# Kernel optimization log

Measured on AMD Instinct MI355X. Metric: run time of the kernel, lower is better.

## Reference

```python
import jax, jax.numpy as jnp
import numpy as np

N = 50000
E = 400000
IN_DIM = 256
H1 = 512
H2 = 128
P_DROP = 0.5


def setup_inputs() -> dict:
    key = jax.random.key(0)
    ks = jax.random.split(key, 8)
    x = jax.random.normal(ks[0], (N, IN_DIM), dtype=jnp.float32)
    edge_index = jax.random.randint(ks[1], (2, E), 0, N, dtype=jnp.int64)
    W1 = jax.random.normal(ks[2], (IN_DIM, H1), dtype=jnp.float32) * (1.0 / np.sqrt(IN_DIM))
    b1 = jnp.zeros((H1,), dtype=jnp.float32)
    W2 = jax.random.normal(ks[3], (H1, H2), dtype=jnp.float32) * (1.0 / np.sqrt(H1))
    b2 = jnp.zeros((H2,), dtype=jnp.float32)
    a = jnp.full((1,), 0.25, dtype=jnp.float32)  # PReLU default init
    mask1 = jax.random.bernoulli(ks[4], 1.0 - P_DROP, (N, H1))
    mask2 = jax.random.bernoulli(ks[5], 1.0 - P_DROP, (N, H2))
    return {"x": x, "edge_index": edge_index, "W1": W1, "b1": b1,
            "W2": W2, "b2": b2, "a": a, "mask1": mask1, "mask2": mask2}


def reference(x, edge_index, W1, b1, W2, b2, a, mask1, mask2):
    n = x.shape[0]
    loop = jnp.arange(n, dtype=edge_index.dtype)
    src = jnp.concatenate([edge_index[0], loop])  # [E+N] with self-loops
    dst = jnp.concatenate([edge_index[1], loop])
    # symmetric normalization: deg^-1/2[src] * deg^-1/2[dst]
    deg = jax.ops.segment_sum(jnp.ones(src.shape[0], x.dtype), dst, num_segments=n)
    dis = jnp.where(deg > 0, jax.lax.rsqrt(jnp.maximum(deg, 1.0)), 0.0)
    norm = dis[src] * dis[dst]  # [E+N]

    scale = 1.0 / (1.0 - P_DROP)

    def gcn_conv(h, W, b):
        h = h @ W                               # dense transform [n, out]
        msg = h[src] * norm[:, None]            # gather + normalize [E+N, out]
        return jax.ops.segment_sum(msg, dst, num_segments=n) + b

    def prelu_dropout(h, mask):
        h = jnp.where(h >= 0, h, a * h)         # PReLU (shared scalar a)
        return jnp.where(mask, h * scale, 0.0)  # dropout p=0.5

    feat1 = prelu_dropout(gcn_conv(x, W1, b1), mask1)
    feat2 = prelu_dropout(gcn_conv(feat1, W2, b2), mask2)
    return feat2
```

## Files before the change

### kernel.cpp

```cpp
#include <hip/hip_runtime.h>
#include <hip/hip_bf16.h>

#define IN_DIM 256
#define H1 512
#define H2 128
#define BM 128
#define BKK 64
#define LDT 72
#define SCAN_CHUNK 4096

typedef unsigned short u16;
typedef unsigned long long u64;
typedef __attribute__((ext_vector_type(8))) short short8;
typedef __attribute__((ext_vector_type(4))) float floatx4;

__device__ __forceinline__ u16 f2bf(float f) {
    union { float f; unsigned u; } c; c.f = f;
    unsigned u = c.u;
    return (u16)((u + 0x7fffu + ((u >> 16) & 1u)) >> 16);
}
__device__ __forceinline__ float bflo(unsigned w) {
    union { unsigned u; float f; } c; c.u = w << 16; return c.f;
}
__device__ __forceinline__ float bfhi(unsigned w) {
    union { unsigned u; float f; } c; c.u = w & 0xffff0000u; return c.f;
}


__global__ __launch_bounds__(256) void prep_kernel(const int4* __restrict__ mask4,
        u64* __restrict__ bits, int total4,
        const int* __restrict__ dstA, int* __restrict__ counts, int E, int n,
        const float* __restrict__ W1, u16* __restrict__ w1t,
        const float* __restrict__ W2, u16* __restrict__ w2t,
        int PB, int HB, int T1B) {
    int b = blockIdx.x;
    if (b < PB) {
        int gid = b * 256 + threadIdx.x;
        int lane = threadIdx.x & 63;
        int4 v = (gid < total4) ? mask4[gid] : make_int4(0, 0, 0, 0);
        u64 b0 = __ballot(v.x != 0);
        u64 b1 = __ballot(v.y != 0);
        u64 b2 = __ballot(v.z != 0);
        u64 b3 = __ballot(v.w != 0);
        u64 sel = (lane == 0) ? b0 : (lane == 1) ? b1 : (lane == 2) ? b2 : b3;
        if (lane < 4 && gid < total4)
            bits[(size_t)(gid >> 6) * 4 + lane] = sel;
    } else if (b < PB + HB) {
        int e = (b - PB) * 256 + threadIdx.x;
        if (e < E) {
            int d = dstA[e];
            if ((unsigned)d < (unsigned)n) atomicAdd(&counts[d], 1);
        }
    } else if (b < PB + HB + T1B) {
        int idx = (b - PB - HB) * 256 + threadIdx.x;
        if (idx < IN_DIM * H1) {
            int k = idx >> 9, c = idx & (H1 - 1);
            w1t[c * IN_DIM + k] = f2bf(W1[idx]);
        }
    } else {
        int idx = (b - PB - HB - T1B) * 256 + threadIdx.x;
        if (idx < H1 * H2) {
            int k = idx >> 7, c = idx & (H2 - 1);
            w2t[c * H1 + k] = f2bf(W2[idx]);
        }
    }
}


__global__ __launch_bounds__(256) void partial_sum_kernel(const int* __restrict__ counts,
        int* __restrict__ partials, int n) {
    int t = threadIdx.x;
    int base = blockIdx.x * SCAN_CHUNK + t * 16;
    int s = 0;
    int m = (base < n) ? min(16, n - base) : 0;
    for (int i = 0; i < m; ++i) s += (counts[base + i] + 1) & ~1;
    __shared__ int red[256];
    red[t] = s;
    __syncthreads();
    for (int off = 128; off > 0; off >>= 1) {
        if (t < off) red[t] += red[t + off];
        __syncthreads();
    }
    if (t == 0) partials[blockIdx.x] = red[0];
}

__global__ void scan_partials_kernel(int* __restrict__ partials, int nb,
                                     unsigned* __restrict__ ts_zero_row) {
    int t = threadIdx.x;
    if (t < 64) ts_zero_row[t] = 0;
    if (t == 0 && blockIdx.x == 0) {
        int run = 0;
        for (int i = 0; i < nb; ++i) { int c = partials[i]; partials[i] = run; run += c; }
        partials[nb] = run;
    }
}

__global__ __launch_bounds__(256) void scan_emit_kernel(const int* __restrict__ counts,
        const int* __restrict__ partials, int* __restrict__ row_start,
        int* __restrict__ cursor, float* __restrict__ dis,
        int* __restrict__ csr, int n, int nb) {
    int t = threadIdx.x;
    int base = blockIdx.x * SCAN_CHUNK + t * 16;
    int cnt[16];
    int s = 0;
    int m = (base < n) ? min(16, n - base) : 0;
    for (int i = 0; i < m; ++i) { cnt[i] = counts[base + i]; s += (cnt[i] + 1) & ~1; }
    __shared__ int red[256];
    red[t] = s;
    __syncthreads();
    for (int off = 1; off < 256; off <<= 1) {
        int v = red[t];
        int vo = (t >= off) ? red[t - off] : 0;
        __syncthreads();
        red[t] = v + vo;
        __syncthreads();
    }
    int run = partials[blockIdx.x] + (t ? red[t - 1] : 0);
    for (int i = 0; i < m; ++i) {
        int c = cnt[i];
        row_start[base + i] = run;
        cursor[base + i] = run;
        dis[base + i] = rsqrtf((float)(c + 1));
        if (c & 1) csr[run + c] = n;
        run += (c + 1) & ~1;
    }
    if (blockIdx.x == 0 && t == 0) row_start[n] = partials[nb];
}

__global__ void scatter_kernel(const int* __restrict__ srcA, const int* __restrict__ dstA,
                               int* __restrict__ cursor, int* __restrict__ csr,
                               int E, int n) {
    int e = blockIdx.x * blockDim.x + threadIdx.x;
    if (e < E) {
        int d = dstA[e];
        int s = srcA[e];
        if ((unsigned)d < (unsigned)n && (unsigned)s < (unsigned)n) {
            int p = atomicAdd(&cursor[d], 1);
            csr[p] = s;
        }
    }
}

__global__ void scale_cast_kernel(const float* __restrict__ x, const float* __restrict__ dis,
                                  u16* __restrict__ xs, int n) {
    int gid = blockIdx.x * blockDim.x + threadIdx.x;
    int total = (n + 1) * (IN_DIM / 4);
    if (gid >= total) return;
    int node = gid >> 6;
    uint2 o = make_uint2(0, 0);
    if (node < n) {
        float4 v = ((const float4*)x)[gid];
        float d = dis[node];
        o.x = (unsigned)f2bf(v.x * d) | ((unsigned)f2bf(v.y * d) << 16);
        o.y = (unsigned)f2bf(v.z * d) | ((unsigned)f2bf(v.w * d) << 16);
    }
    ((uint2*)xs)[gid] = o;
}


__global__ __launch_bounds__(256) void agg1_kernel(const u16* __restrict__ xs,
        const int* __restrict__ row_start, const int* __restrict__ csr,
        const float* __restrict__ dis, u16* __restrict__ aggx, int n) {
    int gid = blockIdx.x * blockDim.x + threadIdx.x;
    int w = gid >> 6, lane = gid & 63;
    if (w >= n) return;
    const uint4* base = (const uint4*)xs;
    int half = lane >> 5, hl = lane & 31;
    float a0 = 0.f, a1 = 0.f, a2 = 0.f, a3 = 0.f, a4 = 0.f, a5 = 0.f, a6 = 0.f, a7 = 0.f;
    if (half == 0) {
        uint4 u = base[(size_t)w * 32 + hl];
        a0 = bflo(u.x); a1 = bfhi(u.x); a2 = bflo(u.y); a3 = bfhi(u.y);
        a4 = bflo(u.z); a5 = bfhi(u.z); a6 = bflo(u.w); a7 = bfhi(u.w);
    }
    int b = row_start[w], e = row_start[w + 1];
    int i = b;
    for (; i + 8 <= e; i += 8) {
        int s0 = csr[i + half],     s1 = csr[i + 2 + half];
        int s2 = csr[i + 4 + half], s3 = csr[i + 6 + half];
        uint4 u0 = base[(size_t)s0 * 32 + hl];
        uint4 u1 = base[(size_t)s1 * 32 + hl];
        uint4 u2 = base[(size_t)s2 * 32 + hl];
        uint4 u3 = base[(size_t)s3 * 32 + hl];
        a0 += (bflo(u0.x) + bflo(u1.x)) + (bflo(u2.x) + bflo(u3.x));
        a1 += (bfhi(u0.x) + bfhi(u1.x)) + (bfhi(u2.x) + bfhi(u3.x));
        a2 += (bflo(u0.y) + bflo(u1.y)) + (bflo(u2.y) + bflo(u3.y));
        a3 += (bfhi(u0.y) + bfhi(u1.y)) + (bfhi(u2.y) + bfhi(u3.y));
        a4 += (bflo(u0.z) + bflo(u1.z)) + (bflo(u2.z) + bflo(u3.z));
        a5 += (bfhi(u0.z) + bfhi(u1.z)) + (bfhi(u2.z) + bfhi(u3.z));
        a6 += (bflo(u0.w) + bflo(u1.w)) + (bflo(u2.w) + bflo(u3.w));
        a7 += (bfhi(u0.w) + bfhi(u1.w)) + (bfhi(u2.w) + bfhi(u3.w));
    }
    for (; i < e; i += 2) {
        int s = csr[i + half];
        uint4 u = base[(size_t)s * 32 + hl];
        a0 += bflo(u.x); a1 += bfhi(u.x); a2 += bflo(u.y); a3 += bfhi(u.y);
        a4 += bflo(u.z); a5 += bfhi(u.z); a6 += bflo(u.w); a7 += bfhi(u.w);
    }
    a0 += __shfl_xor(a0, 32); a1 += __shfl_xor(a1, 32);
    a2 += __shfl_xor(a2, 32); a3 += __shfl_xor(a3, 32);
    a4 += __shfl_xor(a4, 32); a5 += __shfl_xor(a5, 32);
    a6 += __shfl_xor(a6, 32); a7 += __shfl_xor(a7, 32);
    if (half == 0) {
        float dd = dis[w];
        uint4 o;
        o.x = (unsigned)f2bf(a0 * dd) | ((unsigned)f2bf(a1 * dd) << 16);
        o.y = (unsigned)f2bf(a2 * dd) | ((unsigned)f2bf(a3 * dd) << 16);
        o.z = (unsigned)f2bf(a4 * dd) | ((unsigned)f2bf(a5 * dd) << 16);
        o.w = (unsigned)f2bf(a6 * dd) | ((unsigned)f2bf(a7 * dd) << 16);
        ((uint4*)aggx)[(size_t)w * 32 + hl] = o;
    }
}


__global__ __launch_bounds__(256) void gemm1_kernel(const u16* __restrict__ A,
        const u16* __restrict__ Bt, const float* __restrict__ bias,
        const float* __restrict__ a_p, const u64* __restrict__ mbits,
        u16* __restrict__ out, int M) {
    const int K = IN_DIM;
    __shared__ __align__(16) u16 As[BM * LDT];
    __shared__ __align__(16) u16 Bs[BM * LDT];
    int tid = threadIdx.x;
    int wave = tid >> 6, lane = tid & 63;
    int quad = lane >> 4, l16 = lane & 15;
    int wm = wave & 1, wn = wave >> 1;
    int m0 = blockIdx.x * BM, n0 = blockIdx.y * BM;

    floatx4 acc[4][4];
#pragma unroll
    for (int i = 0; i < 4; i++)
#pragma unroll
        for (int j = 0; j < 4; j++) acc[i][j] = (floatx4){0.f, 0.f, 0.f, 0.f};

    for (int k0 = 0; k0 < K; k0 += BKK) {
        __syncthreads();
#pragma unroll
        for (int u = tid; u < 1024; u += 256) {
            int row = u >> 3, seg = u & 7;
            uint4 av = make_uint4(0, 0, 0, 0);
            int gr = m0 + row;
            if (gr < M) av = *(const uint4*)&A[(size_t)gr * K + k0 + seg * 8];
            *(uint4*)&As[row * LDT + seg * 8] = av;
            uint4 bv = *(const uint4*)&Bt[(size_t)(n0 + row) * K + k0 + seg * 8];
            *(uint4*)&Bs[row * LDT + seg * 8] = bv;
        }
        __syncthreads();
        short8 bf8[4][2];
#pragma unroll
        for (int i = 0; i < 4; i++)
#pragma unroll
            for (int ks = 0; ks < 2; ks++)
                bf8[i][ks] = *(const short8*)&Bs[(wn * 64 + i * 16 + l16) * LDT + ks * 32 + quad * 8];
#pragma unroll
        for (int mt = 0; mt < 4; mt++) {
            short8 af0 = *(const short8*)&As[(wm * 64 + mt * 16 + l16) * LDT + quad * 8];
            short8 af1 = *(const short8*)&As[(wm * 64 + mt * 16 + l16) * LDT + 32 + quad * 8];
#pragma unroll
            for (int nt = 0; nt < 4; nt++) {
                acc[mt][nt] = __builtin_amdgcn_mfma_f32_16x16x32_bf16(
                    af0, bf8[nt][0], acc[mt][nt], 0, 0, 0);
                acc[mt][nt] = __builtin_amdgcn_mfma_f32_16x16x32_bf16(
                    af1, bf8[nt][1], acc[mt][nt], 0, 0, 0);
            }
        }
    }

    u64* mb = (u64*)As;
    __syncthreads();
    for (int u = tid; u < BM * 4; u += 256) {
        int row = u >> 2, j = u & 3;
        int gr = m0 + row;
        u64 val = 0;
        if (gr < M) val = mbits[(size_t)gr * 8 + (n0 >> 8) * 4 + j];
        mb[row * 5 + j] = val;
    }
    __syncthreads();

    float alpha = a_p[0];
#pragma unroll
    for (int mt = 0; mt < 4; mt++) {
#pragma unroll
        for (int r = 0; r < 4; r++) {
            int lr = wm * 64 + mt * 16 + quad * 4 + r;
            int row = m0 + lr;
            if (row >= M) continue;
#pragma unroll
            for (int nt = 0; nt < 4; nt++) {
                int c64 = nt * 16 + l16;
                int col = n0 + wn * 64 + c64;
                float v = acc[mt][nt][r] + bias[col];
                v = (v >= 0.f) ? v : alpha * v;
                u64 w = mb[lr * 5 + (l16 & 3)];
                int bit = ((n0 >> 2) + wn * 16 + nt * 4 + (l16 >> 2)) & 63;
                v = ((w >> bit) & 1ull) ? v * 2.0f : 0.0f;
                out[(size_t)row * H1 + col] = f2bf(v);
            }
        }
    }
}


__global__ __launch_bounds__(256) void gemm2_kernel(const u16* __restrict__ A,
        const u16* __restrict__ Bt, const float* __restrict__ dis,
        u16* __restrict__ out, int M) {
    const int K = H1;
    __shared__ __align__(16) u16 As[64 * LDT];
    __shared__ __align__(16) u16 Bs[128 * LDT];
    int tid = threadIdx.x;
    int wave = tid >> 6, lane = tid & 63;
    int quad = lane >> 4, l16 = lane & 15;
    int wm = wave & 1, wn = wave >> 1;
    int m0 = blockIdx.x * 64;

    floatx4 acc[2][4];
#pragma unroll
    for (int i = 0; i < 2; i++)
#pragma unroll
        for (int j = 0; j < 4; j++) acc[i][j] = (floatx4){0.f, 0.f, 0.f, 0.f};

    for (int k0 = 0; k0 < K; k0 += BKK) {
        __syncthreads();
#pragma unroll
        for (int u = tid; u < 1536; u += 256) {
            if (u < 512) {
                int row = u >> 3, seg = u & 7;
                uint4 av = make_uint4(0, 0, 0, 0);
                int gr = m0 + row;
                if (gr < M) av = *(const uint4*)&A[(size_t)gr * K + k0 + seg * 8];
                *(uint4*)&As[row * LDT + seg * 8] = av;
            } else {
                int v2 = u - 512;
                int row = v2 >> 3, seg = v2 & 7;
                uint4 bv = *(const uint4*)&Bt[(size_t)row * K + k0 + seg * 8];
                *(uint4*)&Bs[row * LDT + seg * 8] = bv;
            }
        }
        __syncthreads();
        short8 bf8[4][2];
#pragma unroll
        for (int i = 0; i < 4; i++)
#pragma unroll
            for (int ks = 0; ks < 2; ks++)
                bf8[i][ks] = *(const short8*)&Bs[(wn * 64 + i * 16 + l16) * LDT + ks * 32 + quad * 8];
#pragma unroll
        for (int mt = 0; mt < 2; mt++) {
            short8 af0 = *(const short8*)&As[(wm * 32 + mt * 16 + l16) * LDT + quad * 8];
            short8 af1 = *(const short8*)&As[(wm * 32 + mt * 16 + l16) * LDT + 32 + quad * 8];
#pragma unroll
            for (int nt = 0; nt < 4; nt++) {
                acc[mt][nt] = __builtin_amdgcn_mfma_f32_16x16x32_bf16(
                    af0, bf8[nt][0], acc[mt][nt], 0, 0, 0);
                acc[mt][nt] = __builtin_amdgcn_mfma_f32_16x16x32_bf16(
                    af1, bf8[nt][1], acc[mt][nt], 0, 0, 0);
            }
        }
    }

#pragma unroll
    for (int mt = 0; mt < 2; mt++) {
#pragma unroll
        for (int r = 0; r < 4; r++) {
            int row = m0 + wm * 32 + mt * 16 + quad * 4 + r;
            if (row >= M) continue;
            float dd = dis[row];
#pragma unroll
            for (int nt = 0; nt < 4; nt++) {
                int col = wn * 64 + nt * 16 + l16;
                out[(size_t)row * H2 + col] = f2bf(acc[mt][nt][r] * dd);
            }
        }
    }
}


__global__ __launch_bounds__(256) void agg2_kernel(const u16* __restrict__ ts,
        const int* __restrict__ row_start, const int* __restrict__ csr,
        const float* __restrict__ dis, const float* __restrict__ b2,
        const float* __restrict__ a_p, const int* __restrict__ mask,
        float* __restrict__ out, int n) {
    int gid = blockIdx.x * blockDim.x + threadIdx.x;
    int w = gid >> 6, lane = gid & 63;
    if (w >= n) return;
    const uint2* base = (const uint2*)ts;
    int half = lane >> 5, hl = lane & 31;
    float a0 = 0.f, a1 = 0.f, a2 = 0.f, a3 = 0.f;
    if (half == 0) {
        uint2 u = base[(size_t)w * 32 + hl];
        a0 = bflo(u.x); a1 = bfhi(u.x); a2 = bflo(u.y); a3 = bfhi(u.y);
    }
    int b = row_start[w], e = row_start[w + 1];
    int i = b;
    for (; i + 8 <= e; i += 8) {
        int s0 = csr[i + half],     s1 = csr[i + 2 + half];
        int s2 = csr[i + 4 + half], s3 = csr[i + 6 + half];
        uint2 u0 = base[(size_t)s0 * 32 + hl];
        uint2 u1 = base[(size_t)s1 * 32 + hl];
        uint2 u2 = base[(size_t)s2 * 32 + hl];
        uint2 u3 = base[(size_t)s3 * 32 + hl];
        a0 += (bflo(u0.x) + bflo(u1.x)) + (bflo(u2.x) + bflo(u3.x));
        a1 += (bfhi(u0.x) + bfhi(u1.x)) + (bfhi(u2.x) + bfhi(u3.x));
        a2 += (bflo(u0.y) + bflo(u1.y)) + (bflo(u2.y) + bflo(u3.y));
        a3 += (bfhi(u0.y) + bfhi(u1.y)) + (bfhi(u2.y) + bfhi(u3.y));
    }
    for (; i < e; i += 2) {
        int s = csr[i + half];
        uint2 u = base[(size_t)s * 32 + hl];
        a0 += bflo(u.x); a1 += bfhi(u.x); a2 += bflo(u.y); a3 += bfhi(u.y);
    }
    a0 += __shfl_xor(a0, 32); a1 += __shfl_xor(a1, 32);
    a2 += __shfl_xor(a2, 32); a3 += __shfl_xor(a3, 32);
    if (half == 0) {
        float dd = dis[w];
        float alpha = a_p[0];
        float4 bb = ((const float4*)b2)[hl];
        float v0 = dd * a0 + bb.x;
        float v1 = dd * a1 + bb.y;
        float v2 = dd * a2 + bb.z;
        float v3 = dd * a3 + bb.w;
        v0 = (v0 >= 0.f) ? v0 : alpha * v0;
        v1 = (v1 >= 0.f) ? v1 : alpha * v1;
        v2 = (v2 >= 0.f) ? v2 : alpha * v2;
        v3 = (v3 >= 0.f) ? v3 : alpha * v3;
        int4 m = ((const int4*)mask)[(size_t)w * 32 + hl];
        v0 = m.x ? v0 * 2.f : 0.f;
        v1 = m.y ? v1 * 2.f : 0.f;
        v2 = m.z ? v2 * 2.f : 0.f;
        v3 = m.w ? v3 * 2.f : 0.f;
        ((float4*)out)[(size_t)w * 32 + hl] = make_float4(v0, v1, v2, v3);
    }
}


extern "C" void kernel_launch(void* const* d_in, const int* in_sizes, int n_in,
                              void* d_out, int out_size, void* d_ws, size_t ws_size,
                              hipStream_t stream) {
    const float* x  = (const float*)d_in[0];
    const int* ei   = (const int*)d_in[1];
    const float* W1 = (const float*)d_in[2];
    const float* b1 = (const float*)d_in[3];
    const float* W2 = (const float*)d_in[4];
    const float* b2 = (const float*)d_in[5];
    const float* ap = (const float*)d_in[6];
    const int* mask1 = (const int*)d_in[7];
    const int* mask2 = (const int*)d_in[8];

    int n = in_sizes[0] / IN_DIM;
    int E = in_sizes[1] / 2;
    const int* srcA = ei;
    const int* dstA = ei + E;

    char* p = (char*)d_ws;
    auto alloc = [&](size_t bytes) {
        char* r = p;
        p += (bytes + 255) & ~(size_t)255;
        return r;
    };
    u16* feat1     = (u16*)alloc((size_t)n * H1 * 2);
    u16* xs        = feat1;
    u16* ts        = (u16*)alloc((size_t)(n + 1) * H2 * 2);
    u64* bits1     = (u64*)ts;
    u16* w1t       = (u16*)alloc((size_t)IN_DIM * H1 * 2);
    u16* w2t       = (u16*)alloc((size_t)H1 * H2 * 2);
    float* dis     = (float*)alloc((size_t)n * 4);
    int* counts    = (int*)alloc((size_t)n * 4);
    int* cursor    = (int*)alloc((size_t)n * 4);
    int* row_start = (int*)alloc(((size_t)n + 1) * 4);
    int* csr       = (int*)alloc(((size_t)E + n + 64) * 4);
    int nscan = (n + SCAN_CHUNK - 1) / SCAN_CHUNK;
    int* partials  = (int*)alloc(((size_t)nscan + 1) * 4);
    u16* aggx      = (u16*)d_out;
    if ((size_t)(p - (char*)d_ws) > ws_size) return;

    const int tpb = 256;
    int total4 = n * H1 / 4;
    int PB = (total4 + tpb - 1) / tpb;
    int HB = (E + tpb - 1) / tpb;
    int T1B = (IN_DIM * H1 + tpb - 1) / tpb;
    int T2B = (H1 * H2 + tpb - 1) / tpb;
    hipMemsetAsync(counts, 0, (size_t)n * 4, stream);
    prep_kernel<<<PB + HB + T1B + T2B, tpb, 0, stream>>>((const int4*)mask1, bits1, total4,
        dstA, counts, E, n, W1, w1t, W2, w2t, PB, HB, T1B);
    partial_sum_kernel<<<nscan, tpb, 0, stream>>>(counts, partials, n);
    scan_partials_kernel<<<1, 64, 0, stream>>>(partials, nscan,
        (unsigned*)(ts + (size_t)n * H2));
    scan_emit_kernel<<<nscan, tpb, 0, stream>>>(counts, partials, row_start, cursor, dis,
                                                csr, n, nscan);
    scatter_kernel<<<(E + tpb - 1) / tpb, tpb, 0, stream>>>(srcA, dstA, cursor, csr, E, n);
    scale_cast_kernel<<<(((n + 1) * (IN_DIM / 4)) + tpb - 1) / tpb, tpb, 0, stream>>>(x, dis, xs, n);
    agg1_kernel<<<(n * 64 + tpb - 1) / tpb, tpb, 0, stream>>>(xs, row_start, csr, dis, aggx, n);
    dim3 g1((n + BM - 1) / BM, H1 / BM);
    gemm1_kernel<<<g1, tpb, 0, stream>>>(aggx, w1t, b1, ap, bits1, feat1, n);
    dim3 g2((n + 63) / 64, 1);
    gemm2_kernel<<<g2, tpb, 0, stream>>>(feat1, w2t, dis, ts, n);
    agg2_kernel<<<(n * 64 + tpb - 1) / tpb, tpb, 0, stream>>>(ts, row_start, csr, dis, b2, ap,
                                                              mask2, (float*)d_out, n);
}
```

Baseline: 408.4 us.

## Load GEMM MFMA fragments directly from global memory instead of LDS staging

```diff
diff --git a/kernel.cpp b/kernel.cpp
--- a/kernel.cpp
+++ b/kernel.cpp
@@ -5,8 +5,6 @@
 #define H1 512
 #define H2 128
 #define BM 128
-#define BKK 64
-#define LDT 72
 #define SCAN_CHUNK 4096
 
 typedef unsigned short u16;
@@ -217,55 +215,13 @@
         const float* __restrict__ a_p, const u64* __restrict__ mbits,
         u16* __restrict__ out, int M) {
     const int K = IN_DIM;
-    __shared__ __align__(16) u16 As[BM * LDT];
-    __shared__ __align__(16) u16 Bs[BM * LDT];
+    __shared__ u64 mb[BM * 5];
     int tid = threadIdx.x;
     int wave = tid >> 6, lane = tid & 63;
     int quad = lane >> 4, l16 = lane & 15;
     int wm = wave & 1, wn = wave >> 1;
     int m0 = blockIdx.x * BM, n0 = blockIdx.y * BM;
 
-    floatx4 acc[4][4];
-#pragma unroll
-    for (int i = 0; i < 4; i++)
-#pragma unroll
-        for (int j = 0; j < 4; j++) acc[i][j] = (floatx4){0.f, 0.f, 0.f, 0.f};
-
-    for (int k0 = 0; k0 < K; k0 += BKK) {
-        __syncthreads();
-#pragma unroll
-        for (int u = tid; u < 1024; u += 256) {
-            int row = u >> 3, seg = u & 7;
-            uint4 av = make_uint4(0, 0, 0, 0);
-            int gr = m0 + row;
-            if (gr < M) av = *(const uint4*)&A[(size_t)gr * K + k0 + seg * 8];
-            *(uint4*)&As[row * LDT + seg * 8] = av;
-            uint4 bv = *(const uint4*)&Bt[(size_t)(n0 + row) * K + k0 + seg * 8];
-            *(uint4*)&Bs[row * LDT + seg * 8] = bv;
-        }
-        __syncthreads();
-        short8 bf8[4][2];
-#pragma unroll
-        for (int i = 0; i < 4; i++)
-#pragma unroll
-            for (int ks = 0; ks < 2; ks++)
-                bf8[i][ks] = *(const short8*)&Bs[(wn * 64 + i * 16 + l16) * LDT + ks * 32 + quad * 8];
-#pragma unroll
-        for (int mt = 0; mt < 4; mt++) {
-            short8 af0 = *(const short8*)&As[(wm * 64 + mt * 16 + l16) * LDT + quad * 8];
-            short8 af1 = *(const short8*)&As[(wm * 64 + mt * 16 + l16) * LDT + 32 + quad * 8];
-#pragma unroll
-            for (int nt = 0; nt < 4; nt++) {
-                acc[mt][nt] = __builtin_amdgcn_mfma_f32_16x16x32_bf16(
-                    af0, bf8[nt][0], acc[mt][nt], 0, 0, 0);
-                acc[mt][nt] = __builtin_amdgcn_mfma_f32_16x16x32_bf16(
-                    af1, bf8[nt][1], acc[mt][nt], 0, 0, 0);
-            }
-        }
-    }
-
-    u64* mb = (u64*)As;
-    __syncthreads();
     for (int u = tid; u < BM * 4; u += 256) {
         int row = u >> 2, j = u & 3;
         int gr = m0 + row;
@@ -273,8 +229,48 @@
         if (gr < M) val = mbits[(size_t)gr * 8 + (n0 >> 8) * 4 + j];
         mb[row * 5 + j] = val;
     }
+
+    floatx4 acc[4][4];
+#pragma unroll
+    for (int i = 0; i < 4; i++)
+#pragma unroll
+        for (int j = 0; j < 4; j++) acc[i][j] = (floatx4){0.f, 0.f, 0.f, 0.f};
+
+    const u16* aptr[4];
+#pragma unroll
+    for (int mt = 0; mt < 4; mt++) {
+        int row = m0 + wm * 64 + mt * 16 + l16;
+        if (row >= M) row = M - 1;
+        aptr[mt] = A + (size_t)row * K + quad * 8;
+    }
+    const u16* bptr[4];
+#pragma unroll
+    for (int i = 0; i < 4; i++)
+        bptr[i] = Bt + (size_t)(n0 + wn * 64 + i * 16 + l16) * K + quad * 8;
+
+#pragma unroll
+    for (int k0 = 0; k0 < K; k0 += 64) {
+        short8 bf[4][2];
+#pragma unroll
+        for (int i = 0; i < 4; i++) {
+            bf[i][0] = *(const short8*)(bptr[i] + k0);
+            bf[i][1] = *(const short8*)(bptr[i] + k0 + 32);
+        }
+#pragma unroll
+        for (int mt = 0; mt < 4; mt++) {
+            short8 af0 = *(const short8*)(aptr[mt] + k0);
+            short8 af1 = *(const short8*)(aptr[mt] + k0 + 32);
+#pragma unroll
+            for (int nt = 0; nt < 4; nt++) {
+                acc[mt][nt] = __builtin_amdgcn_mfma_f32_16x16x32_bf16(
+                    af0, bf[nt][0], acc[mt][nt], 0, 0, 0);
+                acc[mt][nt] = __builtin_amdgcn_mfma_f32_16x16x32_bf16(
+                    af1, bf[nt][1], acc[mt][nt], 0, 0, 0);
+            }
+        }
+    }
+
     __syncthreads();
-
     float alpha = a_p[0];
 #pragma unroll
     for (int mt = 0; mt < 4; mt++) {
@@ -303,8 +299,6 @@
         const u16* __restrict__ Bt, const float* __restrict__ dis,
         u16* __restrict__ out, int M) {
     const int K = H1;
-    __shared__ __align__(16) u16 As[64 * LDT];
-    __shared__ __align__(16) u16 Bs[128 * LDT];
     int tid = threadIdx.x;
     int wave = tid >> 6, lane = tid & 63;
     int quad = lane >> 4, l16 = lane & 15;
@@ -317,40 +311,36 @@
 #pragma unroll
         for (int j = 0; j < 4; j++) acc[i][j] = (floatx4){0.f, 0.f, 0.f, 0.f};
 
-    for (int k0 = 0; k0 < K; k0 += BKK) {
-        __syncthreads();
-#pragma unroll
-        for (int u = tid; u < 1536; u += 256) {
-            if (u < 512) {
-                int row = u >> 3, seg = u & 7;
-                uint4 av = make_uint4(0, 0, 0, 0);
-                int gr = m0 + row;
-                if (gr < M) av = *(const uint4*)&A[(size_t)gr * K + k0 + seg * 8];
-                *(uint4*)&As[row * LDT + seg * 8] = av;
-            } else {
-                int v2 = u - 512;
-                int row = v2 >> 3, seg = v2 & 7;
-                uint4 bv = *(const uint4*)&Bt[(size_t)row * K + k0 + seg * 8];
-                *(uint4*)&Bs[row * LDT + seg * 8] = bv;
-            }
-        }
-        __syncthreads();
-        short8 bf8[4][2];
-#pragma unroll
-        for (int i = 0; i < 4; i++)
-#pragma unroll
-            for (int ks = 0; ks < 2; ks++)
-                bf8[i][ks] = *(const short8*)&Bs[(wn * 64 + i * 16 + l16) * LDT + ks * 32 + quad * 8];
+    const u16* aptr[2];
+#pragma unroll
+    for (int mt = 0; mt < 2; mt++) {
+        int row = m0 + wm * 32 + mt * 16 + l16;
+        if (row >= M) row = M - 1;
+        aptr[mt] = A + (size_t)row * K + quad * 8;
+    }
+    const u16* bptr[4];
+#pragma unroll
+    for (int i = 0; i < 4; i++)
+        bptr[i] = Bt + (size_t)(wn * 64 + i * 16 + l16) * K + quad * 8;
+
+#pragma unroll 2
+    for (int k0 = 0; k0 < K; k0 += 64) {
+        short8 bf[4][2];
+#pragma unroll
+        for (int i = 0; i < 4; i++) {
+            bf[i][0] = *(const short8*)(bptr[i] + k0);
+            bf[i][1] = *(const short8*)(bptr[i] + k0 + 32);
+        }
 #pragma unroll
         for (int mt = 0; mt < 2; mt++) {
-            short8 af0 = *(const short8*)&As[(wm * 32 + mt * 16 + l16) * LDT + quad * 8];
-            short8 af1 = *(const short8*)&As[(wm * 32 + mt * 16 + l16) * LDT + 32 + quad * 8];
+            short8 af0 = *(const short8*)(aptr[mt] + k0);
+            short8 af1 = *(const short8*)(aptr[mt] + k0 + 32);
 #pragma unroll
             for (int nt = 0; nt < 4; nt++) {
                 acc[mt][nt] = __builtin_amdgcn_mfma_f32_16x16x32_bf16(
-                    af0, bf8[nt][0], acc[mt][nt], 0, 0, 0);
+                    af0, bf[nt][0], acc[mt][nt], 0, 0, 0);
                 acc[mt][nt] = __builtin_amdgcn_mfma_f32_16x16x32_bf16(
-                    af1, bf8[nt][1], acc[mt][nt], 0, 0, 0);
+                    af1, bf[nt][1], acc[mt][nt], 0, 0, 0);
             }
         }
     }
```

New measurement: 450.6 us. 10.3% more time.
